# Kernel tuning notes

Hardware: AMD Instinct MI355X
Metric: run time of the kernel (lower is better)

Reference implementation:

```python
import jax, jax.numpy as jnp
import numpy as np

N_NODES = 10000
N_EDGES = 320000
K_STEPS = 2          # max_diffusion_step
N_SUPPORTS = 2
C_IN = 64
C_OUT = 64
BATCH = 64
NUM_MATRICES = K_STEPS * N_SUPPORTS + 1  # 5


def setup_inputs() -> dict:
    key = jax.random.key(0)
    k_x, k_v, k_t, k_b, k_r, k_c = jax.random.split(key, 6)
    x = jax.random.normal(k_x, (BATCH, N_NODES, C_IN), dtype=jnp.float32)
    # edge values scaled ~1/avg_degree so row sums are O(1), like a random-walk matrix
    edge_vals = jax.random.uniform(k_v, (N_SUPPORTS, N_EDGES), dtype=jnp.float32) / 32.0
    Theta = jax.random.normal(k_t, (NUM_MATRICES * C_IN, C_OUT), dtype=jnp.float32) * 0.05
    bias = jax.random.normal(k_b, (C_OUT,), dtype=jnp.float32) * 0.01
    edge_rows = jax.random.randint(k_r, (N_SUPPORTS, N_EDGES), 0, N_NODES, dtype=jnp.int32)
    edge_cols = jax.random.randint(k_c, (N_SUPPORTS, N_EDGES), 0, N_NODES, dtype=jnp.int32)
    return {"x": x, "edge_vals": edge_vals, "Theta": Theta, "bias": bias,
            "edge_rows": edge_rows, "edge_cols": edge_cols}


def _spmm(rows, cols, vals, m, n):
    # sparse [n,n] @ dense [n, d] via gather + segment_sum
    return jax.ops.segment_sum(vals[:, None] * m[cols], rows, num_segments=n)


def reference(x, edge_vals, Theta, bias, edge_rows, edge_cols):
    b, n, c = x.shape
    # Faithful to source: raw reshape (n, c*b) of a (b,n,c) tensor (row-major)
    x0 = x.reshape(n, c * b)
    xs = [x0]
    for s in range(N_SUPPORTS):
        rows, cols, vals = edge_rows[s], edge_cols[s], edge_vals[s]
        x_km1, x_km2 = x0, x0
        x1 = _spmm(rows, cols, vals, x0, n)
        xs.append(x1)
        x_km1, x_km2 = x1, x0
        for _ in range(2, K_STEPS + 1):
            x2 = 2.0 * _spmm(rows, cols, vals, x_km1, n) - x_km2
            xs.append(x2)
            x_km1, x_km2 = x2, x_km1
    xcat = jnp.stack(xs, axis=0)                      # (M, n, c*b)
    xcat = xcat.reshape(len(xs), n, c, b)             # (M, n, c, b)
    xcat = xcat.transpose(3, 1, 2, 0)                 # (b, n, c, M)
    xcat = xcat.reshape(b, n, c * len(xs))            # (b, n, c*M)
    out = jnp.matmul(xcat, Theta) + bias              # (b, n, c_out)
    return out
```

## Files before the change

kernel.cpp:

```cpp
#include <hip/hip_runtime.h>
#include <stdint.h>
#include <stddef.h>

#define NN 10000
#define NE 320000
#define NSUP 2
#define CB 4096
#define RPS 10016
#define NCHUNK 32
#define CHUNK_B 256
#define PEPAD 400016

typedef unsigned int uint32;
typedef unsigned short u16;
typedef __attribute__((ext_vector_type(8))) short bf16x8;
typedef __attribute__((ext_vector_type(8))) u16 u16x8;
typedef __attribute__((ext_vector_type(4))) float f32x4;

__device__ __forceinline__ float bf2f(u16 u) {
    union { unsigned int i; float f; } v; v.i = ((unsigned int)u) << 16; return v.f;
}
__device__ __forceinline__ u16 f2bf(float f) {
    union { float f; unsigned int i; } v; v.f = f;
    unsigned int u = v.i;
    return (u16)((u + 0x7fffu + ((u >> 16) & 1u)) >> 16);
}

__global__ __launch_bounds__(256) void k_transpose(const float* __restrict__ x,
                                                   u16* __restrict__ xT) {
    __shared__ float tile[4160];
    const int row = blockIdx.x;
    const int tid = threadIdx.x;
    const f32x4* src = (const f32x4*)(x + (size_t)row * CB);
    #pragma unroll
    for (int q = 0; q < 4; ++q) {
        f32x4 v = src[tid + q * 256];
        int j0 = (tid + q * 256) * 4;
        #pragma unroll
        for (int r = 0; r < 4; ++r) {
            int j = j0 + r;
            tile[j + (j >> 6)] = v[r];
        }
    }
    __syncthreads();
    u16x8 o0, o1;
    #pragma unroll
    for (int jj = 0; jj < 16; ++jj) {
        int j = tid * 16 + jj;
        int b = j >> 6, c = j & 63;
        u16 t = f2bf(tile[c * 65 + b]);
        if (jj < 8) o0[jj] = t; else o1[jj - 8] = t;
    }
    u16x8* dst = (u16x8*)(xT + (size_t)row * CB + tid * 16);
    dst[0] = o0; dst[1] = o1;
}

__global__ __launch_bounds__(256) void k_zero(int* __restrict__ p, int n) {
    int i = blockIdx.x * 256 + threadIdx.x;
    if (i < n) p[i] = 0;
}

__global__ __launch_bounds__(256) void k_hist(const int* __restrict__ rows,
                                              int* __restrict__ counts) {
    int g = blockIdx.x * 256 + threadIdx.x;
    if (g >= NSUP * NE) return;
    int s = g / NE;
    atomicAdd(&counts[s * RPS + rows[g]], 1);
}

__global__ __launch_bounds__(1024) void k_scan(const int* __restrict__ counts,
                                               int* __restrict__ rowptr,
                                               int* __restrict__ cursor) {
    const int s = blockIdx.x;
    const int tid = threadIdx.x;
    __shared__ int buf[1024];
    __shared__ int carry_s;
    if (tid == 0) carry_s = 0;
    __syncthreads();
    for (int base = 0; base < NN; base += 1024) {
        int i = base + tid;
        int v = (i < NN) ? ((counts[s * RPS + i] + 7) & ~7) : 0;
        buf[tid] = v;
        __syncthreads();
        for (int off = 1; off < 1024; off <<= 1) {
            int t = (tid >= off) ? buf[tid - off] : 0;
            __syncthreads();
            buf[tid] += t;
            __syncthreads();
        }
        int carry = carry_s;
        int excl = carry + buf[tid] - v;
        if (i < NN) { rowptr[s * RPS + i] = excl; cursor[s * RPS + i] = excl; }
        __syncthreads();
        if (tid == 1023) carry_s = carry + buf[1023];
        __syncthreads();
    }
    if (tid == 0) rowptr[s * RPS + NN] = carry_s;
}

__global__ __launch_bounds__(256) void k_scatter(const int* __restrict__ rows,
                                                 const int* __restrict__ cols,
                                                 const float* __restrict__ vals,
                                                 int* __restrict__ cursor,
                                                 uint2* __restrict__ pedges) {
    int g = blockIdx.x * 256 + threadIdx.x;
    if (g >= NSUP * NE) return;
    int s = g / NE;
    int r = rows[g];
    int pos = atomicAdd(&cursor[s * RPS + r], 1);
    uint2 p;
    p.x = (unsigned int)cols[g];
    p.y = __float_as_uint(vals[g]);
    pedges[(size_t)s * PEPAD + pos] = p;
}

__global__ __launch_bounds__(256) void k_theta(const float* __restrict__ Theta,
                                               u16* __restrict__ thetaFrag) {
    int idx = blockIdx.x * 256 + threadIdx.x;
    if (idx >= 20480) return;
    int j = idx & 7;
    int lane = (idx >> 3) & 63;
    int ct = (idx >> 9) & 3;
    int ks = idx >> 11;
    int kp = ks * 32 + ((lane >> 4) << 3) + j;
    int m = kp >> 6, c = kp & 63;
    int co = ct * 16 + (lane & 15);
    thetaFrag[idx] = f2bf(Theta[(c * 5 + m) * 64 + co]);
}

#define GATHER8(M)                                                              \
    _Pragma("unroll")                                                           \
    for (int j = 0; j < 8; ++j)                                                 \
        u[j] = *(const uint32*)(srcb + (((M)[j].x << 13) + cb));

#define PREFETCH8(M, blk)                                                       \
    {                                                                           \
        const uint2* pn_ = pe + (size_t)(blk) * 8;                              \
        _Pragma("unroll")                                                       \
        for (int j = 0; j < 8; ++j) (M)[j] = pn_[j];                            \
    }

#define FMA8(M)                                                                 \
    _Pragma("unroll")                                                           \
    for (int j = 0; j < 8; ++j) {                                               \
        float v_ = __uint_as_float((M)[j].y);                                   \
        a0 = fmaf(v_, __uint_as_float(u[j] << 16), a0);                         \
        a1 = fmaf(v_, __uint_as_float(u[j] & 0xffff0000u), a1);                 \
    }

__device__ __forceinline__ void spmm_core(const char* __restrict__ srcb,
                                          const uint2* __restrict__ pe,
                                          int nblk, uint32 cb,
                                          float& a0, float& a1) {
    uint2 ma[8], mb[8];
    uint32 u[8];
    PREFETCH8(ma, 0)
    int b = 0;
    for (; b + 2 <= nblk; b += 2) {
        GATHER8(ma)
        PREFETCH8(mb, b + 1)
        FMA8(ma)
        GATHER8(mb)
        PREFETCH8(ma, b + 2)
        FMA8(mb)
    }
    if (b < nblk) {
        GATHER8(ma)
        FMA8(ma)
    }
}

__global__ __launch_bounds__(256) void k_spmm1(const u16* __restrict__ src,
                                               u16* __restrict__ dst0,
                                               u16* __restrict__ dst1,
                                               const int* __restrict__ rowptr,
                                               const uint2* __restrict__ pedges) {
    const int bx = blockIdx.x;
    const int chunk = bx / (2 * (NN / 4));
    const int r2 = bx - chunk * (2 * (NN / 4));
    const int s = r2 & 1;
    const int quad = r2 >> 1;
    const int wave = threadIdx.x >> 6, lane = threadIdx.x & 63;
    const int row = quad * 4 + wave;
    const uint32 cb = (uint32)chunk * CHUNK_B + (uint32)lane * 4;
    const int* rp = rowptr + s * RPS;
    const int e0 = __builtin_amdgcn_readfirstlane(rp[row]);
    const int e1 = __builtin_amdgcn_readfirstlane(rp[row + 1]);
    const uint2* pe = pedges + (size_t)s * PEPAD + e0;
    float a0 = 0.f, a1 = 0.f;
    spmm_core((const char*)src, pe, (e1 - e0) >> 3, cb, a0, a1);
    u16* dst = s ? dst1 : dst0;
    uint32 o = (uint32)f2bf(a0) | ((uint32)f2bf(a1) << 16);
    __builtin_nontemporal_store(o, (uint32*)((char*)dst + (size_t)row * (CB * 2) + cb));
}

__global__ __launch_bounds__(256) void k_spmm2(const u16* __restrict__ src,
                                               const u16* __restrict__ aux,
                                               u16* __restrict__ dst,
                                               const int* __restrict__ rowptr,
                                               const uint2* __restrict__ pedges) {
    const int bx = blockIdx.x;
    const int chunk = bx / (NN / 4);
    const int quad = bx - chunk * (NN / 4);
    const int wave = threadIdx.x >> 6, lane = threadIdx.x & 63;
    const int row = quad * 4 + wave;
    const uint32 cb = (uint32)chunk * CHUNK_B + (uint32)lane * 4;
    const int e0 = __builtin_amdgcn_readfirstlane(rowptr[row]);
    const int e1 = __builtin_amdgcn_readfirstlane(rowptr[row + 1]);
    const uint2* pe = pedges + e0;
    float a0 = 0.f, a1 = 0.f;
    spmm_core((const char*)src, pe, (e1 - e0) >> 3, cb, a0, a1);
    const size_t rowoff = (size_t)row * (CB * 2) + cb;
    uint32 av = __builtin_nontemporal_load((const uint32*)((const char*)aux + rowoff));
    float c0 = 2.f * a0 - __uint_as_float(av << 16);
    float c1 = 2.f * a1 - __uint_as_float(av & 0xffff0000u);
    uint32 o = (uint32)f2bf(c0) | ((uint32)f2bf(c1) << 16);
    __builtin_nontemporal_store(o, (uint32*)((char*)dst + rowoff));
}

__global__ __launch_bounds__(256) void k_gemm(const u16* __restrict__ mats,
                                              const u16* __restrict__ thetaFrag,
                                              const float* __restrict__ bias,
                                              float* __restrict__ out) {
    __shared__ u16 th[20480];
    const int tid = threadIdx.x;
    #pragma unroll
    for (int q = 0; q < 10; ++q) {
        int idx = tid * 8 + q * 2048;
        *(u16x8*)&th[idx] = *(const u16x8*)&thetaFrag[idx];
    }
    __syncthreads();
    const int wave = tid >> 6, lane = tid & 63;
    const int node = blockIdx.x * 4 + wave;
    const int l15 = lane & 15, lhi = lane >> 4;

    f32x4 acc[4][4];
    #pragma unroll
    for (int ct = 0; ct < 4; ++ct) {
        float bv = bias[ct * 16 + l15];
        #pragma unroll
        for (int bt = 0; bt < 4; ++bt) {
            acc[bt][ct][0] = bv; acc[bt][ct][1] = bv; acc[bt][ct][2] = bv; acc[bt][ct][3] = bv;
        }
    }
    #pragma unroll
    for (int ks = 0; ks < 10; ++ks) {
        const int m = ks >> 1;
        const int c0 = ((ks & 1) << 5) + (lhi << 3);
        const u16* mbase = mats + (size_t)m * ((size_t)NN * CB) + (size_t)node * CB;
        bf16x8 af[4];
        #pragma unroll
        for (int bt = 0; bt < 4; ++bt)
            af[bt] = *(const bf16x8*)(mbase + (bt * 16 + l15) * 64 + c0);
        #pragma unroll
        for (int ct = 0; ct < 4; ++ct) {
            bf16x8 bf = *(const bf16x8*)&th[((ks * 4 + ct) * 64 + lane) * 8];
            #pragma unroll
            for (int bt = 0; bt < 4; ++bt)
                acc[bt][ct] = __builtin_amdgcn_mfma_f32_16x16x32_bf16(af[bt], bf, acc[bt][ct], 0, 0, 0);
        }
    }
    #pragma unroll
    for (int bt = 0; bt < 4; ++bt)
        #pragma unroll
        for (int ct = 0; ct < 4; ++ct)
            #pragma unroll
            for (int r = 0; r < 4; ++r) {
                int b = bt * 16 + lhi * 4 + r;
                int co = ct * 16 + l15;
                out[(size_t)b * (NN * 64) + (size_t)node * 64 + co] = acc[bt][ct][r];
            }
}

extern "C" void kernel_launch(void* const* d_in, const int* in_sizes, int n_in,
                              void* d_out, int out_size, void* d_ws, size_t ws_size,
                              hipStream_t stream) {
    const float* x         = (const float*)d_in[0];
    const float* edge_vals = (const float*)d_in[1];
    const float* Theta     = (const float*)d_in[2];
    const float* bias      = (const float*)d_in[3];
    const int*   edge_rows = (const int*)d_in[4];
    const int*   edge_cols = (const int*)d_in[5];
    float* out = (float*)d_out;

    uint8_t* ws = (uint8_t*)d_ws;
    const size_t MAT_E = (size_t)NN * CB;
    const size_t MAT_B = MAT_E * 2;

    u16* mats      = (u16*)ws;
    u16* thetaFrag = (u16*)(ws + 5 * MAT_B);
    uint8_t* p = ws + 5 * MAT_B + 40960;
    int* counts = (int*)p;  p += (size_t)NSUP * RPS * 4;
    int* rowptr = (int*)p;  p += (size_t)NSUP * RPS * 4;
    int* cursor = (int*)p;  p += (size_t)NSUP * RPS * 4;
    p = (uint8_t*)(((uintptr_t)p + 255) & ~(uintptr_t)255);
    uint2* pedges = (uint2*)p;

    u16* m0 = mats;
    u16* m1 = mats + MAT_E;
    u16* m2 = mats + 2 * MAT_E;
    u16* m3 = mats + 3 * MAT_E;
    u16* m4 = mats + 4 * MAT_E;

    k_transpose<<<NN, 256, 0, stream>>>(x, m0);
    k_zero<<<(NSUP * RPS + 255) / 256, 256, 0, stream>>>(counts, NSUP * RPS);
    k_zero<<<(NSUP * PEPAD * 2 + 255) / 256, 256, 0, stream>>>((int*)pedges, NSUP * PEPAD * 2);
    k_hist<<<(NSUP * NE) / 256, 256, 0, stream>>>(edge_rows, counts);
    k_scan<<<NSUP, 1024, 0, stream>>>(counts, rowptr, cursor);
    k_scatter<<<(NSUP * NE) / 256, 256, 0, stream>>>(edge_rows, edge_cols, edge_vals,
                                                     cursor, pedges);
    k_theta<<<80, 256, 0, stream>>>(Theta, thetaFrag);

    k_spmm1<<<NCHUNK * (NN / 4) * 2, 256, 0, stream>>>(m0, m1, m3, rowptr, pedges);
    k_spmm2<<<NCHUNK * (NN / 4), 256, 0, stream>>>(m1, m0, m2, rowptr, pedges);
    k_spmm2<<<NCHUNK * (NN / 4), 256, 0, stream>>>(m3, m0, m4, rowptr + RPS, pedges + PEPAD);

    k_gemm<<<NN / 4, 256, 0, stream>>>(mats, thetaFrag, bias, out);
}
```

Baseline: 951.1 us.

## Widen SpMM gathers to 8 bytes per lane and merge second-step launches

Each lane now gathers 4 bf16 values (8 bytes) per edge instead of 2, with chunk width doubled and chunk count halved. Each edge record fetch is amortized over twice as many columns, and the number of SpMM blocks drops. The two per-support second-step SpMM launches are fused into one grid covering both supports, removing a launch and letting the work overlap. This costs more registers per thread and halves the number of waves in flight, which may reduce latency hiding for the random gathers.

```diff
diff --git a/kernel.cpp b/kernel.cpp
--- a/kernel.cpp
+++ b/kernel.cpp
@@ -7,8 +7,8 @@
 #define NSUP 2
 #define CB 4096
 #define RPS 10016
-#define NCHUNK 32
-#define CHUNK_B 256
+#define NCHUNK 16
+#define CHUNK_B 512
 #define PEPAD 400016
 
 typedef unsigned int uint32;
@@ -16,6 +16,7 @@
 typedef __attribute__((ext_vector_type(8))) short bf16x8;
 typedef __attribute__((ext_vector_type(8))) u16 u16x8;
 typedef __attribute__((ext_vector_type(4))) float f32x4;
+typedef __attribute__((ext_vector_type(2))) uint32 u32x2;
 
 __device__ __forceinline__ float bf2f(u16 u) {
     union { unsigned int i; float f; } v; v.i = ((unsigned int)u) << 16; return v.f;
@@ -128,10 +129,10 @@
     thetaFrag[idx] = f2bf(Theta[(c * 5 + m) * 64 + co]);
 }
 
-#define GATHER8(M)                                                              \
+#define GATHER8(G, M)                                                           \
     _Pragma("unroll")                                                           \
     for (int j = 0; j < 8; ++j)                                                 \
-        u[j] = *(const uint32*)(srcb + (((M)[j].x << 13) + cb));
+        (G)[j] = *(const u32x2*)(srcb + (((M)[j].x << 13) + cb));
 
 #define PREFETCH8(M, blk)                                                       \
     {                                                                           \
@@ -140,33 +141,36 @@
         for (int j = 0; j < 8; ++j) (M)[j] = pn_[j];                            \
     }
 
-#define FMA8(M)                                                                 \
+#define FMA8(G, M)                                                              \
     _Pragma("unroll")                                                           \
     for (int j = 0; j < 8; ++j) {                                               \
         float v_ = __uint_as_float((M)[j].y);                                   \
-        a0 = fmaf(v_, __uint_as_float(u[j] << 16), a0);                         \
-        a1 = fmaf(v_, __uint_as_float(u[j] & 0xffff0000u), a1);                 \
+        a0 = fmaf(v_, __uint_as_float((G)[j].x << 16), a0);                     \
+        a1 = fmaf(v_, __uint_as_float((G)[j].x & 0xffff0000u), a1);             \
+        a2 = fmaf(v_, __uint_as_float((G)[j].y << 16), a2);                     \
+        a3 = fmaf(v_, __uint_as_float((G)[j].y & 0xffff0000u), a3);             \
     }
 
 __device__ __forceinline__ void spmm_core(const char* __restrict__ srcb,
                                           const uint2* __restrict__ pe,
                                           int nblk, uint32 cb,
-                                          float& a0, float& a1) {
+                                          float& a0, float& a1,
+                                          float& a2, float& a3) {
     uint2 ma[8], mb[8];
-    uint32 u[8];
+    u32x2 ga[8], gb[8];
     PREFETCH8(ma, 0)
     int b = 0;
     for (; b + 2 <= nblk; b += 2) {
-        GATHER8(ma)
+        GATHER8(ga, ma)
         PREFETCH8(mb, b + 1)
-        FMA8(ma)
-        GATHER8(mb)
+        FMA8(ga, ma)
+        GATHER8(gb, mb)
         PREFETCH8(ma, b + 2)
-        FMA8(mb)
+        FMA8(gb, mb)
     }
     if (b < nblk) {
-        GATHER8(ma)
-        FMA8(ma)
+        GATHER8(ga, ma)
+        FMA8(ga, ma)
     }
 }
 
@@ -182,40 +186,55 @@
     const int quad = r2 >> 1;
     const int wave = threadIdx.x >> 6, lane = threadIdx.x & 63;
     const int row = quad * 4 + wave;
-    const uint32 cb = (uint32)chunk * CHUNK_B + (uint32)lane * 4;
+    const uint32 cb = (uint32)chunk * CHUNK_B + (uint32)lane * 8;
     const int* rp = rowptr + s * RPS;
     const int e0 = __builtin_amdgcn_readfirstlane(rp[row]);
     const int e1 = __builtin_amdgcn_readfirstlane(rp[row + 1]);
     const uint2* pe = pedges + (size_t)s * PEPAD + e0;
-    float a0 = 0.f, a1 = 0.f;
-    spmm_core((const char*)src, pe, (e1 - e0) >> 3, cb, a0, a1);
+    float a0 = 0.f, a1 = 0.f, a2 = 0.f, a3 = 0.f;
+    spmm_core((const char*)src, pe, (e1 - e0) >> 3, cb, a0, a1, a2, a3);
     u16* dst = s ? dst1 : dst0;
-    uint32 o = (uint32)f2bf(a0) | ((uint32)f2bf(a1) << 16);
-    __builtin_nontemporal_store(o, (uint32*)((char*)dst + (size_t)row * (CB * 2) + cb));
-}
-
-__global__ __launch_bounds__(256) void k_spmm2(const u16* __restrict__ src,
+    u32x2 o;
+    o.x = (uint32)f2bf(a0) | ((uint32)f2bf(a1) << 16);
+    o.y = (uint32)f2bf(a2) | ((uint32)f2bf(a3) << 16);
+    __builtin_nontemporal_store(o, (u32x2*)((char*)dst + (size_t)row * (CB * 2) + cb));
+}
+
+__global__ __launch_bounds__(256) void k_spmm2(const u16* __restrict__ src0,
+                                               const u16* __restrict__ src1,
                                                const u16* __restrict__ aux,
-                                               u16* __restrict__ dst,
+                                               u16* __restrict__ dst0,
+                                               u16* __restrict__ dst1,
                                                const int* __restrict__ rowptr,
                                                const uint2* __restrict__ pedges) {
     const int bx = blockIdx.x;
-    const int chunk = bx / (NN / 4);
-    const int quad = bx - chunk * (NN / 4);
+    const int chunk = bx / (2 * (NN / 4));
+    const int r2 = bx - chunk * (2 * (NN / 4));
+    const int s = r2 / (NN / 4);
+    const int quad = r2 - s * (NN / 4);
     const int wave = threadIdx.x >> 6, lane = threadIdx.x & 63;
     const int row = quad * 4 + wave;
-    const uint32 cb = (uint32)chunk * CHUNK_B + (uint32)lane * 4;
-    const int e0 = __builtin_amdgcn_readfirstlane(rowptr[row]);
-    const int e1 = __builtin_amdgcn_readfirstlane(rowptr[row + 1]);
-    const uint2* pe = pedges + e0;
-    float a0 = 0.f, a1 = 0.f;
-    spmm_core((const char*)src, pe, (e1 - e0) >> 3, cb, a0, a1);
+    const uint32 cb = (uint32)chunk * CHUNK_B + (uint32)lane * 8;
+    const int* rp = rowptr + s * RPS;
+    const int e0 = __builtin_amdgcn_readfirstlane(rp[row]);
+    const int e1 = __builtin_amdgcn_readfirstlane(rp[row + 1]);
+    const uint2* pe = pedges + (size_t)s * PEPAD + e0;
+    const char* srcb = (const char*)(s ? src1 : src0);
+    float a0 = 0.f, a1 = 0.f, a2 = 0.f, a3 = 0.f;
+    spmm_core(srcb, pe, (e1 - e0) >> 3, cb, a0, a1, a2, a3);
     const size_t rowoff = (size_t)row * (CB * 2) + cb;
-    uint32 av = __builtin_nontemporal_load((const uint32*)((const char*)aux + rowoff));
-    float c0 = 2.f * a0 - __uint_as_float(av << 16);
-    float c1 = 2.f * a1 - __uint_as_float(av & 0xffff0000u);
-    uint32 o = (uint32)f2bf(c0) | ((uint32)f2bf(c1) << 16);
-    __builtin_nontemporal_store(o, (uint32*)((char*)dst + rowoff));
+    u32x2 av = __builtin_nontemporal_load((const u32x2*)((const char*)aux + rowoff));
+    u32x2 o;
+    {
+        float c0 = 2.f * a0 - __uint_as_float(av.x << 16);
+        float c1 = 2.f * a1 - __uint_as_float(av.x & 0xffff0000u);
+        float c2 = 2.f * a2 - __uint_as_float(av.y << 16);
+        float c3 = 2.f * a3 - __uint_as_float(av.y & 0xffff0000u);
+        o.x = (uint32)f2bf(c0) | ((uint32)f2bf(c1) << 16);
+        o.y = (uint32)f2bf(c2) | ((uint32)f2bf(c3) << 16);
+    }
+    u16* dst = s ? dst1 : dst0;
+    __builtin_nontemporal_store(o, (u32x2*)((char*)dst + rowoff));
 }
 
 __global__ __launch_bounds__(256) void k_gemm(const u16* __restrict__ mats,
@@ -312,8 +331,8 @@
     k_theta<<<80, 256, 0, stream>>>(Theta, thetaFrag);
 
     k_spmm1<<<NCHUNK * (NN / 4) * 2, 256, 0, stream>>>(m0, m1, m3, rowptr, pedges);
-    k_spmm2<<<NCHUNK * (NN / 4), 256, 0, stream>>>(m1, m0, m2, rowptr, pedges);
-    k_spmm2<<<NCHUNK * (NN / 4), 256, 0, stream>>>(m3, m0, m4, rowptr + RPS, pedges + PEPAD);
+    k_spmm2<<<NCHUNK * (NN / 4) * 2, 256, 0, stream>>>(m1, m3, m0, m2, m4,
+                                                       rowptr, pedges);
 
     k_gemm<<<NN / 4, 256, 0, stream>>>(mats, thetaFrag, bias, out);
 }
```

Measured after the change: 1.017 ms. 6.9% more time.
